# Performance work log

Measured on AMD Instinct MI355X. Metric: run time of the kernel, lower is better.

## Reference

```python
import jax, jax.numpy as jnp
import numpy as np

B, N, D, H = 16, 512, 512, 8
DK = D // H
SCALE = DK ** (-0.5)
NEG = -9.0e15
LN_EPS = 1e-5


def setup_inputs() -> dict:
    key = jax.random.key(0)
    ks = jax.random.split(key, 16)
    std = 1.0 / np.sqrt(D)
    x = jax.random.normal(ks[0], (B, N, D), jnp.float32)
    adj = jax.random.randint(ks[1], (B, N, N), 0, 2).astype(jnp.float32)
    # weights stored [in, out] (y = x @ W + b)
    def lin(k, fin, fout):
        return jax.random.normal(k, (fin, fout), jnp.float32) * (1.0 / np.sqrt(fin))
    return {
        "x": x,
        "adj": adj,
        "W_w": lin(ks[2], D, D), "W_b": jnp.zeros((D,), jnp.float32),
        "ln_g": jnp.ones((D,), jnp.float32), "ln_b": jnp.zeros((D,), jnp.float32),
        "Wq": lin(ks[3], D, D), "bq": jnp.zeros((D,), jnp.float32),
        "Wk": lin(ks[4], D, D), "bk": jnp.zeros((D,), jnp.float32),
        "Wv": lin(ks[5], D, D), "bv": jnp.zeros((D,), jnp.float32),
        "Wo": lin(ks[6], D, D), "bo": jnp.zeros((D,), jnp.float32),
        "gate_w": lin(ks[7], 2 * D, 1), "gate_b": jnp.zeros((1,), jnp.float32),
        "use_adj": 1,
    }


def _layernorm(h, g, b):
    mu = jnp.mean(h, axis=-1, keepdims=True)
    var = jnp.mean(jnp.square(h - mu), axis=-1, keepdims=True)
    return (h - mu) * jax.lax.rsqrt(var + LN_EPS) * g + b


def _forward(x, adj, W_w, W_b, ln_g, ln_b, Wq, bq, Wk, bk, Wv, bv, Wo, bo, gate_w, gate_b, use_adj):
    h = x @ W_w + W_b                      # [B,N,D]
    h = _layernorm(h, ln_g, ln_b)
    q = (h @ Wq + bq).reshape(B, N, H, DK)
    k = (h @ Wk + bk).reshape(B, N, H, DK)
    v = (h @ Wv + bv).reshape(B, N, H, DK)
    scores = jnp.einsum('bqhd,bkhd->bhqk', q * SCALE, k)   # [B,H,N,N]
    if use_adj:
        a = adj[:, None, :, :]
        scores = jnp.where(a > 0, scores, NEG) * a
    attn = jax.nn.softmax(scores, axis=-1)
    ctx = jnp.einsum('bhqk,bkhd->bqhd', attn, v).reshape(B, N, D)
    h2 = jax.nn.relu(ctx @ Wo + bo)        # dropout = identity (eval)
    coeff = jax.nn.sigmoid(jnp.concatenate([x, h2], axis=-1) @ gate_w + gate_b)  # [B,N,1]
    return coeff * x + (1.0 - coeff) * h2


def reference(x, adj, W_w, W_b, ln_g, ln_b, Wq, bq, Wk, bk, Wv, bv, Wo, bo, gate_w, gate_b, use_adj):
    return _forward(x, adj, W_w, W_b, ln_g, ln_b, Wq, bq, Wk, bk, Wv, bv, Wo, bo, gate_w, gate_b, use_adj)
```

## Files before the change

### kernel.cpp

```cpp
#include <hip/hip_runtime.h>
#include <stdint.h>


typedef __bf16 bf16_t;
typedef __bf16 bf16x8 __attribute__((ext_vector_type(8)));
typedef __bf16 bf16x4 __attribute__((ext_vector_type(4)));
typedef float  f32x4  __attribute__((ext_vector_type(4)));

#define B_   16
#define N_   512
#define D_   512
#define H_   8
#define DK_  64
#define BN_  8192

__global__ __launch_bounds__(256) void k_transpose_w(const float* __restrict__ W,
                                                     bf16_t* __restrict__ Wt) {
  __shared__ float tile[32][33];
  const int kb = blockIdx.x * 32, nb = blockIdx.y * 32;
  const int tx = threadIdx.x, ty = threadIdx.y;
#pragma unroll
  for (int i = ty; i < 32; i += 8)
    tile[i][tx] = W[(long)(kb + i) * D_ + nb + tx];
  __syncthreads();
#pragma unroll
  for (int i = ty; i < 32; i += 8)
    Wt[(long)(nb + i) * D_ + kb + tx] = (bf16_t)tile[tx][i];
}

__global__ __launch_bounds__(256) void k_transpose_v(const bf16_t* __restrict__ vB,
                                                     bf16_t* __restrict__ vT) {
  __shared__ bf16_t tile[64][72];
  const int tt = blockIdx.x & 7;
  const int bh = blockIdx.x >> 3;
  const int b = bh >> 3, h = bh & 7;
  const int t = threadIdx.x;
  const int sr = t >> 2, sc = (t & 3) * 16;
  {
    const bf16_t* src = vB + (long)(b * N_ + tt * 64 + sr) * D_ + h * DK_ + sc;
    *(uint4*)&tile[sr][sc]     = *(const uint4*)src;
    *(uint4*)&tile[sr][sc + 8] = *(const uint4*)(src + 8);
  }
  __syncthreads();
  bf16_t* dst = vT + ((long)bh * DK_ + sr) * N_ + tt * 64 + sc;
#pragma unroll
  for (int i = 0; i < 16; ++i) dst[i] = tile[sc + i][sr];
}

template <int AMODE, int OMODE>
__global__ __launch_bounds__(256) void k_gemm(const void* __restrict__ Ap,
                                              const bf16_t* __restrict__ Bt,
                                              const float* __restrict__ bias,
                                              void* __restrict__ outp,
                                              float outScale) {
  __shared__ bf16_t As[64][40];
  __shared__ bf16_t Bs[64][40];
  const int t = threadIdx.x;
  const int m0 = blockIdx.x * 64;
  const int n0 = blockIdx.y * 64;
  const int wave = t >> 6, lane = t & 63;
  const int quad = lane >> 4, l16 = lane & 15;
  const int wm = (wave >> 1) * 32, wn = (wave & 1) * 32;
  const int sr = t >> 2, sc = (t & 3) * 8;

  f32x4 acc[2][2] = {};

  const long aoff = (long)(m0 + sr) * D_;
  const long boff = (long)(n0 + sr) * D_;

  for (int k0 = 0; k0 < D_; k0 += 32) {
    __syncthreads();
    if (AMODE == 0) {
      const float* Af = (const float*)Ap;
      float4 f0 = *(const float4*)&Af[aoff + k0 + sc];
      float4 f1 = *(const float4*)&Af[aoff + k0 + sc + 4];
      bf16x8 a8;
      a8[0] = (bf16_t)f0.x; a8[1] = (bf16_t)f0.y; a8[2] = (bf16_t)f0.z; a8[3] = (bf16_t)f0.w;
      a8[4] = (bf16_t)f1.x; a8[5] = (bf16_t)f1.y; a8[6] = (bf16_t)f1.z; a8[7] = (bf16_t)f1.w;
      *(bf16x8*)&As[sr][sc] = a8;
    } else {
      *(uint4*)&As[sr][sc] = *(const uint4*)((const bf16_t*)Ap + aoff + k0 + sc);
    }
    *(uint4*)&Bs[sr][sc] = *(const uint4*)&Bt[boff + k0 + sc];
    __syncthreads();

    bf16x8 af0 = *(const bf16x8*)&As[wm + l16][quad * 8];
    bf16x8 af1 = *(const bf16x8*)&As[wm + 16 + l16][quad * 8];
    bf16x8 bf0 = *(const bf16x8*)&Bs[wn + l16][quad * 8];
    bf16x8 bf1 = *(const bf16x8*)&Bs[wn + 16 + l16][quad * 8];
    acc[0][0] = __builtin_amdgcn_mfma_f32_16x16x32_bf16(af0, bf0, acc[0][0], 0, 0, 0);
    acc[0][1] = __builtin_amdgcn_mfma_f32_16x16x32_bf16(af0, bf1, acc[0][1], 0, 0, 0);
    acc[1][0] = __builtin_amdgcn_mfma_f32_16x16x32_bf16(af1, bf0, acc[1][0], 0, 0, 0);
    acc[1][1] = __builtin_amdgcn_mfma_f32_16x16x32_bf16(af1, bf1, acc[1][1], 0, 0, 0);
  }

#pragma unroll
  for (int ti = 0; ti < 2; ++ti)
#pragma unroll
    for (int tj = 0; tj < 2; ++tj) {
      const int n = n0 + wn + tj * 16 + l16;
      const float bv = bias[n];
#pragma unroll
      for (int r = 0; r < 4; ++r) {
        const int m = m0 + wm + ti * 16 + quad * 4 + r;
        float v = (acc[ti][tj][r] + bv) * outScale;
        if (OMODE == 2) v = fmaxf(v, 0.0f);
        if (OMODE == 1) ((bf16_t*)outp)[(long)m * D_ + n] = (bf16_t)v;
        else            ((float*)outp)[(long)m * D_ + n]  = v;
      }
    }
}

__global__ __launch_bounds__(256) void k_layernorm(const float* __restrict__ hp,
                                                   const float* __restrict__ g,
                                                   const float* __restrict__ bb,
                                                   bf16_t* __restrict__ out) {
  const int row = blockIdx.x * 4 + (threadIdx.x >> 6);
  const int lane = threadIdx.x & 63;
  const float* hr = hp + (long)row * D_;
  float v[8];
  *(float4*)&v[0] = ((const float4*)hr)[lane * 2];
  *(float4*)&v[4] = ((const float4*)hr)[lane * 2 + 1];
  float s = 0.f;
#pragma unroll
  for (int i = 0; i < 8; ++i) s += v[i];
#pragma unroll
  for (int o = 32; o > 0; o >>= 1) s += __shfl_xor(s, o, 64);
  const float mu = s * (1.0f / 512.0f);
  float vs = 0.f;
#pragma unroll
  for (int i = 0; i < 8; ++i) { float d = v[i] - mu; vs += d * d; }
#pragma unroll
  for (int o = 32; o > 0; o >>= 1) vs += __shfl_xor(vs, o, 64);
  const float rstd = rsqrtf(vs * (1.0f / 512.0f) + 1e-5f);
  float gv[8], bv[8];
  *(float4*)&gv[0] = ((const float4*)g)[lane * 2];
  *(float4*)&gv[4] = ((const float4*)g)[lane * 2 + 1];
  *(float4*)&bv[0] = ((const float4*)bb)[lane * 2];
  *(float4*)&bv[4] = ((const float4*)bb)[lane * 2 + 1];
  bf16x8 o8;
#pragma unroll
  for (int i = 0; i < 8; ++i) o8[i] = (bf16_t)((v[i] - mu) * rstd * gv[i] + bv[i]);
  *(bf16x8*)&out[(long)row * D_ + lane * 8] = o8;
}

__global__ __launch_bounds__(256) void k_attn(const bf16_t* __restrict__ qb,
                                              const bf16_t* __restrict__ kb,
                                              const bf16_t* __restrict__ vT,
                                              const float* __restrict__ adj,
                                              const int* __restrict__ use_adj_p,
                                              bf16_t* __restrict__ ctx) {
  __shared__ bf16_t Ks[64][72];
  __shared__ bf16_t Vs[64][72];
  __shared__ bf16_t Ps[4][16][72];
  const int t = threadIdx.x;
  const int w = t >> 6, lane = t & 63;
  const int quad = lane >> 4, l16 = lane & 15;
  const int qt = blockIdx.x & 7;
  const int bh = blockIdx.x >> 3;
  const int b = bh >> 3, h = bh & 7;
  const int q0 = qt * 64;
  const int use_adj = use_adj_p[0];

  const long qoff = (long)(b * N_ + q0 + w * 16 + l16) * D_ + h * DK_ + quad * 8;
  const bf16x8 aq0 = *(const bf16x8*)&qb[qoff];
  const bf16x8 aq1 = *(const bf16x8*)&qb[qoff + 32];

  const int sr = t >> 2, sc = (t & 3) * 16;
  const bf16_t* kbase  = kb + (long)b * N_ * D_ + h * DK_;
  const bf16_t* vtbase = vT + (long)bh * DK_ * N_;
  const float*  adjbase = adj + ((long)b * N_ + q0 + w * 16 + quad * 4) * N_;

  f32x4 accO[4] = {};
  float m_i[4] = {-3.0e38f, -3.0e38f, -3.0e38f, -3.0e38f};
  float l_i[4] = {0.f, 0.f, 0.f, 0.f};

  for (int kt = 0; kt < 8; ++kt) {
    __syncthreads();
    {
      const bf16_t* ksrc = kbase + (long)(kt * 64 + sr) * D_ + sc;
      *(uint4*)&Ks[sr][sc]     = *(const uint4*)ksrc;
      *(uint4*)&Ks[sr][sc + 8] = *(const uint4*)(ksrc + 8);
      const bf16_t* vsrc = vtbase + (long)sr * N_ + kt * 64 + sc;
      *(uint4*)&Vs[sr][sc]     = *(const uint4*)vsrc;
      *(uint4*)&Vs[sr][sc + 8] = *(const uint4*)(vsrc + 8);
    }
    __syncthreads();

    f32x4 s[4];
#pragma unroll
    for (int nt = 0; nt < 4; ++nt) {
      bf16x8 bk0 = *(const bf16x8*)&Ks[nt * 16 + l16][quad * 8];
      bf16x8 bk1 = *(const bf16x8*)&Ks[nt * 16 + l16][quad * 8 + 32];
      f32x4 z = {};
      z = __builtin_amdgcn_mfma_f32_16x16x32_bf16(aq0, bk0, z, 0, 0, 0);
      z = __builtin_amdgcn_mfma_f32_16x16x32_bf16(aq1, bk1, z, 0, 0, 0);
      s[nt] = z;
    }

    if (use_adj) {
#pragma unroll
      for (int nt = 0; nt < 4; ++nt)
#pragma unroll
        for (int r = 0; r < 4; ++r) {
          float a = adjbase[(long)r * N_ + kt * 64 + nt * 16 + l16];
          s[nt][r] = (a > 0.f) ? s[nt][r] : 0.0f;
        }
    }

    float tm[4];
#pragma unroll
    for (int r = 0; r < 4; ++r)
      tm[r] = fmaxf(fmaxf(s[0][r], s[1][r]), fmaxf(s[2][r], s[3][r]));
#pragma unroll
    for (int o = 1; o < 16; o <<= 1)
#pragma unroll
      for (int r = 0; r < 4; ++r) tm[r] = fmaxf(tm[r], __shfl_xor(tm[r], o, 64));
    float al[4];
#pragma unroll
    for (int r = 0; r < 4; ++r) {
      const float mn = fmaxf(m_i[r], tm[r]);
      al[r] = __expf(m_i[r] - mn);
      m_i[r] = mn;
    }
    float rs[4] = {0.f, 0.f, 0.f, 0.f};
#pragma unroll
    for (int nt = 0; nt < 4; ++nt)
#pragma unroll
      for (int r = 0; r < 4; ++r) {
        const float e = __expf(s[nt][r] - m_i[r]);
        s[nt][r] = e;
        rs[r] += e;
      }
#pragma unroll
    for (int o = 1; o < 16; o <<= 1)
#pragma unroll
      for (int r = 0; r < 4; ++r) rs[r] += __shfl_xor(rs[r], o, 64);
#pragma unroll
    for (int r = 0; r < 4; ++r) l_i[r] = l_i[r] * al[r] + rs[r];
#pragma unroll
    for (int nt = 0; nt < 4; ++nt)
#pragma unroll
      for (int r = 0; r < 4; ++r) accO[nt][r] *= al[r];

#pragma unroll
    for (int nt = 0; nt < 4; ++nt)
#pragma unroll
      for (int r = 0; r < 4; ++r)
        Ps[w][quad * 4 + r][nt * 16 + l16] = (bf16_t)s[nt][r];
    __builtin_amdgcn_s_waitcnt(0xC07F);

    bf16x8 ap0 = *(const bf16x8*)&Ps[w][l16][quad * 8];
    bf16x8 ap1 = *(const bf16x8*)&Ps[w][l16][quad * 8 + 32];
#pragma unroll
    for (int nt = 0; nt < 4; ++nt) {
      bf16x8 bv0 = *(const bf16x8*)&Vs[nt * 16 + l16][quad * 8];
      bf16x8 bv1 = *(const bf16x8*)&Vs[nt * 16 + l16][quad * 8 + 32];
      accO[nt] = __builtin_amdgcn_mfma_f32_16x16x32_bf16(ap0, bv0, accO[nt], 0, 0, 0);
      accO[nt] = __builtin_amdgcn_mfma_f32_16x16x32_bf16(ap1, bv1, accO[nt], 0, 0, 0);
    }
  }

  float inv[4];
#pragma unroll
  for (int r = 0; r < 4; ++r) inv[r] = 1.0f / l_i[r];
#pragma unroll
  for (int r = 0; r < 4; ++r) {
    const long orow = (long)(b * N_ + q0 + w * 16 + quad * 4 + r) * D_ + h * DK_;
#pragma unroll
    for (int nt = 0; nt < 4; ++nt)
      ctx[orow + nt * 16 + l16] = (bf16_t)(accO[nt][r] * inv[r]);
  }
}

__global__ __launch_bounds__(256) void k_gate(const float* __restrict__ x,
                                              const float* __restrict__ h2,
                                              const float* __restrict__ gw,
                                              const float* __restrict__ gb,
                                              float* __restrict__ outp) {
  const int row = blockIdx.x * 4 + (threadIdx.x >> 6);
  const int lane = threadIdx.x & 63;
  const long base = (long)row * D_ + lane * 8;
  float xv[8], hv[8], w0[8], w1[8];
  *(float4*)&xv[0] = *(const float4*)&x[base];
  *(float4*)&xv[4] = *(const float4*)&x[base + 4];
  *(float4*)&hv[0] = *(const float4*)&h2[base];
  *(float4*)&hv[4] = *(const float4*)&h2[base + 4];
  *(float4*)&w0[0] = *(const float4*)&gw[lane * 8];
  *(float4*)&w0[4] = *(const float4*)&gw[lane * 8 + 4];
  *(float4*)&w1[0] = *(const float4*)&gw[512 + lane * 8];
  *(float4*)&w1[4] = *(const float4*)&gw[512 + lane * 8 + 4];
  float s = 0.f;
#pragma unroll
  for (int i = 0; i < 8; ++i) s += xv[i] * w0[i] + hv[i] * w1[i];
#pragma unroll
  for (int o = 32; o > 0; o >>= 1) s += __shfl_xor(s, o, 64);
  const float z = s + gb[0];
  const float coeff = 1.0f / (1.0f + __expf(-z));
#pragma unroll
  for (int i = 0; i < 8; ++i)
    outp[base + i] = coeff * xv[i] + (1.0f - coeff) * hv[i];
}

extern "C" void kernel_launch(void* const* d_in, const int* in_sizes, int n_in,
                              void* d_out, int out_size, void* d_ws, size_t ws_size,
                              hipStream_t stream) {
  (void)in_sizes; (void)n_in; (void)out_size; (void)ws_size;
  const float* x    = (const float*)d_in[0];
  const float* adj  = (const float*)d_in[1];
  const float* W_w  = (const float*)d_in[2];
  const float* W_b  = (const float*)d_in[3];
  const float* ln_g = (const float*)d_in[4];
  const float* ln_b = (const float*)d_in[5];
  const float* Wq   = (const float*)d_in[6];
  const float* bq   = (const float*)d_in[7];
  const float* Wk   = (const float*)d_in[8];
  const float* bk   = (const float*)d_in[9];
  const float* Wv   = (const float*)d_in[10];
  const float* bv   = (const float*)d_in[11];
  const float* Wo   = (const float*)d_in[12];
  const float* bo   = (const float*)d_in[13];
  const float* gw   = (const float*)d_in[14];
  const float* gb   = (const float*)d_in[15];
  const int* use_adj = (const int*)d_in[16];

  char* ws = (char*)d_ws;
  size_t off = 0;
  auto alloc = [&](size_t bytes) -> void* {
    void* p = ws + off;
    off += (bytes + 255) & ~(size_t)255;
    return p;
  };
  bf16_t* WtW  = (bf16_t*)alloc((size_t)D_ * D_ * 2);
  bf16_t* WtQ  = (bf16_t*)alloc((size_t)D_ * D_ * 2);
  bf16_t* WtK  = (bf16_t*)alloc((size_t)D_ * D_ * 2);
  bf16_t* WtV  = (bf16_t*)alloc((size_t)D_ * D_ * 2);
  bf16_t* WtO  = (bf16_t*)alloc((size_t)D_ * D_ * 2);
  float*  hPre = (float*)alloc((size_t)BN_ * D_ * 4);
  bf16_t* hB   = (bf16_t*)alloc((size_t)BN_ * D_ * 2);
  bf16_t* qB   = (bf16_t*)alloc((size_t)BN_ * D_ * 2);
  bf16_t* kB   = (bf16_t*)alloc((size_t)BN_ * D_ * 2);
  bf16_t* vB   = (bf16_t*)alloc((size_t)BN_ * D_ * 2);
  bf16_t* vTB  = (bf16_t*)alloc((size_t)BN_ * D_ * 2);
  bf16_t* ctxB = (bf16_t*)alloc((size_t)BN_ * D_ * 2);
  float*  h2   = hPre;

  dim3 tb(32, 8), tg(16, 16);
  k_transpose_w<<<tg, tb, 0, stream>>>(W_w, WtW);
  k_transpose_w<<<tg, tb, 0, stream>>>(Wq, WtQ);
  k_transpose_w<<<tg, tb, 0, stream>>>(Wk, WtK);
  k_transpose_w<<<tg, tb, 0, stream>>>(Wv, WtV);
  k_transpose_w<<<tg, tb, 0, stream>>>(Wo, WtO);

  dim3 gg(BN_ / 64, D_ / 64);
  k_gemm<0, 0><<<gg, 256, 0, stream>>>(x, WtW, W_b, hPre, 1.0f);
  k_layernorm<<<BN_ / 4, 256, 0, stream>>>(hPre, ln_g, ln_b, hB);
  k_gemm<1, 1><<<gg, 256, 0, stream>>>(hB, WtQ, bq, qB, 0.125f);
  k_gemm<1, 1><<<gg, 256, 0, stream>>>(hB, WtK, bk, kB, 1.0f);
  k_gemm<1, 1><<<gg, 256, 0, stream>>>(hB, WtV, bv, vB, 1.0f);
  k_transpose_v<<<B_ * H_ * 8, 256, 0, stream>>>(vB, vTB);
  k_attn<<<B_ * H_ * 8, 256, 0, stream>>>(qB, kB, vTB, adj, use_adj, ctxB);
  k_gemm<1, 2><<<gg, 256, 0, stream>>>(ctxB, WtO, bo, h2, 1.0f);
  k_gate<<<BN_ / 4, 256, 0, stream>>>(x, h2, gw, gb, (float*)d_out);
}
```

Before: 238.0 us.

## Use 128x128 GEMM tiles with direct LDS loads, fuse QKV, byte mask

Replaces the 64x64 GEMM with a 128x128-tile kernel that loads global memory straight into LDS, giving each wave a 4x4 block of MFMA tiles. The Q, K and V projections become one GEMM over a concatenated weight that writes an interleaved qkv buffer. x is cast to bf16 up front, and adj is compacted into a byte mask so attention reads a quarter of the bytes. The goal is more reuse per loaded tile, fewer launches and less memory traffic. The costs are two extra prepass kernels, which read x and adj in full, and an unpadded LDS layout that may cause bank conflicts.

```diff
diff --git a/kernel.cpp b/kernel.cpp
--- a/kernel.cpp
+++ b/kernel.cpp
@@ -14,6 +14,32 @@
 #define DK_  64
 #define BN_  8192
 
+__device__ __forceinline__ void gl2lds16(const void* g, void* l) {
+  __builtin_amdgcn_global_load_lds(
+      (const __attribute__((address_space(1))) void*)g,
+      (__attribute__((address_space(3))) void*)l, 16, 0, 0);
+}
+
+__global__ __launch_bounds__(256) void k_cast_x(const float* __restrict__ x,
+                                                bf16_t* __restrict__ xb) {
+  const long i = ((long)blockIdx.x * 256 + threadIdx.x) * 8;
+  float4 a = *(const float4*)&x[i];
+  float4 b = *(const float4*)&x[i + 4];
+  bf16x8 o;
+  o[0] = (bf16_t)a.x; o[1] = (bf16_t)a.y; o[2] = (bf16_t)a.z; o[3] = (bf16_t)a.w;
+  o[4] = (bf16_t)b.x; o[5] = (bf16_t)b.y; o[6] = (bf16_t)b.z; o[7] = (bf16_t)b.w;
+  *(bf16x8*)&xb[i] = o;
+}
+
+__global__ __launch_bounds__(256) void k_mask(const float* __restrict__ adj,
+                                              uint8_t* __restrict__ mask) {
+  const long i = ((long)blockIdx.x * 256 + threadIdx.x) * 4;
+  float4 a = *(const float4*)&adj[i];
+  uint32_t m = (a.x > 0.f ? 1u : 0u) | (a.y > 0.f ? 1u : 0u) << 8 |
+               (a.z > 0.f ? 1u : 0u) << 16 | (a.w > 0.f ? 1u : 0u) << 24;
+  *(uint32_t*)&mask[i] = m;
+}
+
 __global__ __launch_bounds__(256) void k_transpose_w(const float* __restrict__ W,
                                                      bf16_t* __restrict__ Wt) {
   __shared__ float tile[32][33];
@@ -28,7 +54,7 @@
     Wt[(long)(nb + i) * D_ + kb + tx] = (bf16_t)tile[tx][i];
 }
 
-__global__ __launch_bounds__(256) void k_transpose_v(const bf16_t* __restrict__ vB,
+__global__ __launch_bounds__(256) void k_transpose_v(const bf16_t* __restrict__ qkv,
                                                      bf16_t* __restrict__ vT) {
   __shared__ bf16_t tile[64][72];
   const int tt = blockIdx.x & 7;
@@ -37,7 +63,7 @@
   const int t = threadIdx.x;
   const int sr = t >> 2, sc = (t & 3) * 16;
   {
-    const bf16_t* src = vB + (long)(b * N_ + tt * 64 + sr) * D_ + h * DK_ + sc;
+    const bf16_t* src = qkv + (long)(b * N_ + tt * 64 + sr) * 1536 + 1024 + h * DK_ + sc;
     *(uint4*)&tile[sr][sc]     = *(const uint4*)src;
     *(uint4*)&tile[sr][sc + 8] = *(const uint4*)(src + 8);
   }
@@ -47,68 +73,72 @@
   for (int i = 0; i < 16; ++i) dst[i] = tile[sc + i][sr];
 }
 
-template <int AMODE, int OMODE>
-__global__ __launch_bounds__(256) void k_gemm(const void* __restrict__ Ap,
-                                              const bf16_t* __restrict__ Bt,
-                                              const float* __restrict__ bias,
-                                              void* __restrict__ outp,
-                                              float outScale) {
-  __shared__ bf16_t As[64][40];
-  __shared__ bf16_t Bs[64][40];
+template <int OMODE>
+__global__ __launch_bounds__(256) void k_gemm128(const bf16_t* __restrict__ A,
+                                                 const bf16_t* __restrict__ Bt,
+                                                 const float* __restrict__ b0,
+                                                 const float* __restrict__ b1,
+                                                 const float* __restrict__ b2,
+                                                 float s0, float s1, float s2,
+                                                 void* __restrict__ outp, int ldOut) {
+  __shared__ bf16_t As[128 * 32];
+  __shared__ bf16_t Bs[128 * 32];
   const int t = threadIdx.x;
-  const int m0 = blockIdx.x * 64;
-  const int n0 = blockIdx.y * 64;
-  const int wave = t >> 6, lane = t & 63;
+  const int m0 = blockIdx.x * 128;
+  const int n0 = blockIdx.y * 128;
+  const int w = t >> 6, lane = t & 63;
   const int quad = lane >> 4, l16 = lane & 15;
-  const int wm = (wave >> 1) * 32, wn = (wave & 1) * 32;
-  const int sr = t >> 2, sc = (t & 3) * 8;
-
-  f32x4 acc[2][2] = {};
-
-  const long aoff = (long)(m0 + sr) * D_;
-  const long boff = (long)(n0 + sr) * D_;
-
-  for (int k0 = 0; k0 < D_; k0 += 32) {
+  const int wm = (w >> 1) * 64, wn = (w & 1) * 64;
+
+  const int e0 = t * 8;
+  const int r0 = e0 >> 5, c0 = e0 & 31;
+  const bf16_t* agp0 = A + (long)(m0 + r0) * 512 + c0;
+  const bf16_t* agp1 = agp0 + (long)64 * 512;
+  const bf16_t* bgp0 = Bt + (long)(n0 + r0) * 512 + c0;
+  const bf16_t* bgp1 = bgp0 + (long)64 * 512;
+
+  f32x4 acc[4][4] = {};
+
+  for (int k0 = 0; k0 < 512; k0 += 32) {
     __syncthreads();
-    if (AMODE == 0) {
-      const float* Af = (const float*)Ap;
-      float4 f0 = *(const float4*)&Af[aoff + k0 + sc];
-      float4 f1 = *(const float4*)&Af[aoff + k0 + sc + 4];
-      bf16x8 a8;
-      a8[0] = (bf16_t)f0.x; a8[1] = (bf16_t)f0.y; a8[2] = (bf16_t)f0.z; a8[3] = (bf16_t)f0.w;
-      a8[4] = (bf16_t)f1.x; a8[5] = (bf16_t)f1.y; a8[6] = (bf16_t)f1.z; a8[7] = (bf16_t)f1.w;
-      *(bf16x8*)&As[sr][sc] = a8;
-    } else {
-      *(uint4*)&As[sr][sc] = *(const uint4*)((const bf16_t*)Ap + aoff + k0 + sc);
-    }
-    *(uint4*)&Bs[sr][sc] = *(const uint4*)&Bt[boff + k0 + sc];
+    gl2lds16(agp0 + k0, &As[e0]);
+    gl2lds16(agp1 + k0, &As[e0 + 2048]);
+    gl2lds16(bgp0 + k0, &Bs[e0]);
+    gl2lds16(bgp1 + k0, &Bs[e0 + 2048]);
     __syncthreads();
 
-    bf16x8 af0 = *(const bf16x8*)&As[wm + l16][quad * 8];
-    bf16x8 af1 = *(const bf16x8*)&As[wm + 16 + l16][quad * 8];
-    bf16x8 bf0 = *(const bf16x8*)&Bs[wn + l16][quad * 8];
-    bf16x8 bf1 = *(const bf16x8*)&Bs[wn + 16 + l16][quad * 8];
-    acc[0][0] = __builtin_amdgcn_mfma_f32_16x16x32_bf16(af0, bf0, acc[0][0], 0, 0, 0);
-    acc[0][1] = __builtin_amdgcn_mfma_f32_16x16x32_bf16(af0, bf1, acc[0][1], 0, 0, 0);
-    acc[1][0] = __builtin_amdgcn_mfma_f32_16x16x32_bf16(af1, bf0, acc[1][0], 0, 0, 0);
-    acc[1][1] = __builtin_amdgcn_mfma_f32_16x16x32_bf16(af1, bf1, acc[1][1], 0, 0, 0);
-  }
-
-#pragma unroll
-  for (int ti = 0; ti < 2; ++ti)
-#pragma unroll
-    for (int tj = 0; tj < 2; ++tj) {
-      const int n = n0 + wn + tj * 16 + l16;
-      const float bv = bias[n];
+    bf16x8 af[4], bfr[4];
+#pragma unroll
+    for (int i = 0; i < 4; ++i) {
+      af[i]  = *(const bf16x8*)&As[(wm + i * 16 + l16) * 32 + quad * 8];
+      bfr[i] = *(const bf16x8*)&Bs[(wn + i * 16 + l16) * 32 + quad * 8];
+    }
+#pragma unroll
+    for (int mi = 0; mi < 4; ++mi)
+#pragma unroll
+      for (int ni = 0; ni < 4; ++ni)
+        acc[mi][ni] = __builtin_amdgcn_mfma_f32_16x16x32_bf16(af[mi], bfr[ni],
+                                                              acc[mi][ni], 0, 0, 0);
+  }
+
+  const int seg = n0 >> 9;
+  const float* bias = (seg == 0) ? b0 : (seg == 1) ? b1 : b2;
+  const float scale = (seg == 0) ? s0 : (seg == 1) ? s1 : s2;
+#pragma unroll
+  for (int ni = 0; ni < 4; ++ni) {
+    const int n = n0 + wn + ni * 16 + l16;
+    const float bv = bias[n & 511];
+#pragma unroll
+    for (int mi = 0; mi < 4; ++mi)
 #pragma unroll
       for (int r = 0; r < 4; ++r) {
-        const int m = m0 + wm + ti * 16 + quad * 4 + r;
-        float v = (acc[ti][tj][r] + bv) * outScale;
+        const long m = m0 + wm + mi * 16 + quad * 4 + r;
+        float v = (acc[mi][ni][r] + bv) * scale;
         if (OMODE == 2) v = fmaxf(v, 0.0f);
-        if (OMODE == 1) ((bf16_t*)outp)[(long)m * D_ + n] = (bf16_t)v;
-        else            ((float*)outp)[(long)m * D_ + n]  = v;
+        if (OMODE == 1) ((bf16_t*)outp)[m * ldOut + n] = (bf16_t)v;
+        else            ((float*)outp)[m * ldOut + n]  = v;
       }
-    }
+  }
 }
 
 __global__ __launch_bounds__(256) void k_layernorm(const float* __restrict__ hp,
@@ -144,10 +174,9 @@
   *(bf16x8*)&out[(long)row * D_ + lane * 8] = o8;
 }
 
-__global__ __launch_bounds__(256) void k_attn(const bf16_t* __restrict__ qb,
-                                              const bf16_t* __restrict__ kb,
+__global__ __launch_bounds__(256) void k_attn(const bf16_t* __restrict__ qkv,
                                               const bf16_t* __restrict__ vT,
-                                              const float* __restrict__ adj,
+                                              const uint8_t* __restrict__ mask,
                                               const int* __restrict__ use_adj_p,
                                               bf16_t* __restrict__ ctx) {
   __shared__ bf16_t Ks[64][72];
@@ -162,14 +191,14 @@
   const int q0 = qt * 64;
   const int use_adj = use_adj_p[0];
 
-  const long qoff = (long)(b * N_ + q0 + w * 16 + l16) * D_ + h * DK_ + quad * 8;
-  const bf16x8 aq0 = *(const bf16x8*)&qb[qoff];
-  const bf16x8 aq1 = *(const bf16x8*)&qb[qoff + 32];
+  const long qoff = (long)(b * N_ + q0 + w * 16 + l16) * 1536 + h * DK_ + quad * 8;
+  const bf16x8 aq0 = *(const bf16x8*)&qkv[qoff];
+  const bf16x8 aq1 = *(const bf16x8*)&qkv[qoff + 32];
 
   const int sr = t >> 2, sc = (t & 3) * 16;
-  const bf16_t* kbase  = kb + (long)b * N_ * D_ + h * DK_;
+  const bf16_t* kbase  = qkv + (long)b * N_ * 1536 + 512 + h * DK_;
   const bf16_t* vtbase = vT + (long)bh * DK_ * N_;
-  const float*  adjbase = adj + ((long)b * N_ + q0 + w * 16 + quad * 4) * N_;
+  const uint8_t* mbase = mask + ((long)b * N_ + q0 + w * 16 + quad * 4) * N_;
 
   f32x4 accO[4] = {};
   float m_i[4] = {-3.0e38f, -3.0e38f, -3.0e38f, -3.0e38f};
@@ -178,7 +207,7 @@
   for (int kt = 0; kt < 8; ++kt) {
     __syncthreads();
     {
-      const bf16_t* ksrc = kbase + (long)(kt * 64 + sr) * D_ + sc;
+      const bf16_t* ksrc = kbase + (long)(kt * 64 + sr) * 1536 + sc;
       *(uint4*)&Ks[sr][sc]     = *(const uint4*)ksrc;
       *(uint4*)&Ks[sr][sc + 8] = *(const uint4*)(ksrc + 8);
       const bf16_t* vsrc = vtbase + (long)sr * N_ + kt * 64 + sc;
@@ -203,8 +232,8 @@
       for (int nt = 0; nt < 4; ++nt)
 #pragma unroll
         for (int r = 0; r < 4; ++r) {
-          float a = adjbase[(long)r * N_ + kt * 64 + nt * 16 + l16];
-          s[nt][r] = (a > 0.f) ? s[nt][r] : 0.0f;
+          uint8_t a = mbase[(long)r * N_ + kt * 64 + nt * 16 + l16];
+          s[nt][r] = a ? s[nt][r] : 0.0f;
         }
     }
 
@@ -331,35 +360,38 @@
     off += (bytes + 255) & ~(size_t)255;
     return p;
   };
-  bf16_t* WtW  = (bf16_t*)alloc((size_t)D_ * D_ * 2);
-  bf16_t* WtQ  = (bf16_t*)alloc((size_t)D_ * D_ * 2);
-  bf16_t* WtK  = (bf16_t*)alloc((size_t)D_ * D_ * 2);
-  bf16_t* WtV  = (bf16_t*)alloc((size_t)D_ * D_ * 2);
-  bf16_t* WtO  = (bf16_t*)alloc((size_t)D_ * D_ * 2);
-  float*  hPre = (float*)alloc((size_t)BN_ * D_ * 4);
-  bf16_t* hB   = (bf16_t*)alloc((size_t)BN_ * D_ * 2);
-  bf16_t* qB   = (bf16_t*)alloc((size_t)BN_ * D_ * 2);
-  bf16_t* kB   = (bf16_t*)alloc((size_t)BN_ * D_ * 2);
-  bf16_t* vB   = (bf16_t*)alloc((size_t)BN_ * D_ * 2);
-  bf16_t* vTB  = (bf16_t*)alloc((size_t)BN_ * D_ * 2);
-  bf16_t* ctxB = (bf16_t*)alloc((size_t)BN_ * D_ * 2);
-  float*  h2   = hPre;
+  bf16_t*  WtW   = (bf16_t*)alloc((size_t)D_ * D_ * 2);
+  bf16_t*  WtQKV = (bf16_t*)alloc((size_t)3 * D_ * D_ * 2);
+  bf16_t*  WtO   = (bf16_t*)alloc((size_t)D_ * D_ * 2);
+  bf16_t*  xb    = (bf16_t*)alloc((size_t)BN_ * D_ * 2);
+  uint8_t* mB    = (uint8_t*)alloc((size_t)B_ * N_ * N_);
+  float*   hPre  = (float*)alloc((size_t)BN_ * D_ * 4);
+  bf16_t*  hB    = (bf16_t*)alloc((size_t)BN_ * D_ * 2);
+  bf16_t*  qkv   = (bf16_t*)alloc((size_t)BN_ * 3 * D_ * 2);
+  bf16_t*  vTB   = (bf16_t*)alloc((size_t)BN_ * D_ * 2);
+  bf16_t*  ctxB  = (bf16_t*)alloc((size_t)BN_ * D_ * 2);
+  float*   h2    = hPre;
+
+  k_cast_x<<<BN_ * D_ / 2048, 256, 0, stream>>>(x, xb);
+  k_mask<<<B_ * N_ * N_ / 1024, 256, 0, stream>>>(adj, mB);
 
   dim3 tb(32, 8), tg(16, 16);
   k_transpose_w<<<tg, tb, 0, stream>>>(W_w, WtW);
-  k_transpose_w<<<tg, tb, 0, stream>>>(Wq, WtQ);
-  k_transpose_w<<<tg, tb, 0, stream>>>(Wk, WtK);
-  k_transpose_w<<<tg, tb, 0, stream>>>(Wv, WtV);
+  k_transpose_w<<<tg, tb, 0, stream>>>(Wq, WtQKV);
+  k_transpose_w<<<tg, tb, 0, stream>>>(Wk, WtQKV + (size_t)D_ * D_);
+  k_transpose_w<<<tg, tb, 0, stream>>>(Wv, WtQKV + (size_t)2 * D_ * D_);
   k_transpose_w<<<tg, tb, 0, stream>>>(Wo, WtO);
 
-  dim3 gg(BN_ / 64, D_ / 64);
-  k_gemm<0, 0><<<gg, 256, 0, stream>>>(x, WtW, W_b, hPre, 1.0f);
+  dim3 gh(BN_ / 128, D_ / 128);
+  dim3 gqkv(BN_ / 128, 3 * D_ / 128);
+  k_gemm128<0><<<gh, 256, 0, stream>>>(xb, WtW, W_b, W_b, W_b, 1.f, 1.f, 1.f,
+                                       hPre, D_);
   k_layernorm<<<BN_ / 4, 256, 0, stream>>>(hPre, ln_g, ln_b, hB);
-  k_gemm<1, 1><<<gg, 256, 0, stream>>>(hB, WtQ, bq, qB, 0.125f);
-  k_gemm<1, 1><<<gg, 256, 0, stream>>>(hB, WtK, bk, kB, 1.0f);
-  k_gemm<1, 1><<<gg, 256, 0, stream>>>(hB, WtV, bv, vB, 1.0f);
-  k_transpose_v<<<B_ * H_ * 8, 256, 0, stream>>>(vB, vTB);
-  k_attn<<<B_ * H_ * 8, 256, 0, stream>>>(qB, kB, vTB, adj, use_adj, ctxB);
-  k_gemm<1, 2><<<gg, 256, 0, stream>>>(ctxB, WtO, bo, h2, 1.0f);
+  k_gemm128<1><<<gqkv, 256, 0, stream>>>(hB, WtQKV, bq, bk, bv, 0.125f, 1.f, 1.f,
+                                         qkv, 3 * D_);
+  k_transpose_v<<<B_ * H_ * 8, 256, 0, stream>>>(qkv, vTB);
+  k_attn<<<B_ * H_ * 8, 256, 0, stream>>>(qkv, vTB, mB, use_adj, ctxB);
+  k_gemm128<2><<<gh, 256, 0, stream>>>(ctxB, WtO, bo, bo, bo, 1.f, 1.f, 1.f,
+                                       h2, D_);
   k_gate<<<BN_ / 4, 256, 0, stream>>>(x, h2, gw, gb, (float*)d_out);
 }
```

Measured after the change: 227.7 us. 4.3% less time.
